# Kernel optimization log

Measured on AMD Instinct MI355X. Metric: run time of the kernel, lower is better.

The kernel has to match this reference:

```python
import jax, jax.numpy as jnp
import numpy as np

D = 128      # d_model
H = 8        # nhead
DFF = 256    # dim_feedforward
S = 1000     # num sets
L = 90       # set size
N = S * L    # total tokens (lidar voxels + image patches)
VN = 45000   # voxel_num (lidar tokens)


def _ln(x, g, b, eps=1e-5):
    m = x.mean(-1, keepdims=True)
    v = ((x - m) ** 2).mean(-1, keepdims=True)
    return (x - m) / jnp.sqrt(v + eps) * g + b


def setup_inputs() -> dict:
    key = jax.random.key(0)
    ks = jax.random.split(key, 16)
    p = lambda k, sh: jax.random.normal(k, sh, jnp.float32) * 0.02
    inp = {
        "src": jax.random.normal(ks[0], (N, D), jnp.float32),
        "pos": jax.random.normal(ks[1], (N, D), jnp.float32),
        # every token appears exactly once across all sets (permutation)
        "set_voxel_inds": jax.random.permutation(ks[2], N).reshape(S, L).astype(jnp.int32),
        "set_voxel_masks": jnp.zeros((S, L), bool),
        "voxel_num": VN,
        # nn.MultiheadAttention params
        "in_proj_w": p(ks[3], (3 * D, D)), "in_proj_b": jnp.zeros((3 * D,), jnp.float32),
        "out_w": p(ks[4], (D, D)), "out_b": jnp.zeros((D,), jnp.float32),
        # image-branch FFN + norms
        "lin1_w": p(ks[5], (DFF, D)), "lin1_b": jnp.zeros((DFF,), jnp.float32),
        "lin2_w": p(ks[6], (D, DFF)), "lin2_b": jnp.zeros((D,), jnp.float32),
        "n1_g": jnp.ones((D,), jnp.float32), "n1_b": jnp.zeros((D,), jnp.float32),
        "n2_g": jnp.ones((D,), jnp.float32), "n2_b": jnp.zeros((D,), jnp.float32),
        # lidar-branch FFN + norms (split_ffn=True)
        "l_lin1_w": p(ks[7], (DFF, D)), "l_lin1_b": jnp.zeros((DFF,), jnp.float32),
        "l_lin2_w": p(ks[8], (D, DFF)), "l_lin2_b": jnp.zeros((D,), jnp.float32),
        "ln1_g": jnp.ones((D,), jnp.float32), "ln1_b": jnp.zeros((D,), jnp.float32),
        "ln2_g": jnp.ones((D,), jnp.float32), "ln2_b": jnp.zeros((D,), jnp.float32),
        # encoder-layer output norm
        "enc_g": jnp.ones((D,), jnp.float32), "enc_b": jnp.zeros((D,), jnp.float32),
    }
    return inp


def reference(src, pos, set_voxel_inds, set_voxel_masks, voxel_num,
              in_proj_w, in_proj_b, out_w, out_b,
              lin1_w, lin1_b, lin2_w, lin2_b, n1_g, n1_b, n2_g, n2_b,
              l_lin1_w, l_lin1_b, l_lin2_w, l_lin2_b, ln1_g, ln1_b, ln2_g, ln2_b,
              enc_g, enc_b):
    identity = src
    Sx, Lx = set_voxel_inds.shape
    d = src.shape[-1]
    dh = d // H

    # ---- gather sets ----
    sf = src[set_voxel_inds]              # [S, L, D]
    sp = pos[set_voxel_inds]              # [S, L, D]
    q = sf + sp
    k = sf + sp
    v = sf

    # ---- nn.MultiheadAttention (batch_first, eval mode) ----
    qp = q @ in_proj_w[:d].T + in_proj_b[:d]
    kp = k @ in_proj_w[d:2 * d].T + in_proj_b[d:2 * d]
    vp = v @ in_proj_w[2 * d:].T + in_proj_b[2 * d:]
    qh = qp.reshape(Sx, Lx, H, dh)
    kh = kp.reshape(Sx, Lx, H, dh)
    vh = vp.reshape(Sx, Lx, H, dh)
    scale = 1.0 / np.sqrt(dh).astype(np.float32)
    scores = jnp.einsum('sqhd,skhd->shqk', qh, kh) * scale
    scores = scores + jnp.where(set_voxel_masks[:, None, None, :], -1e9, 0.0)
    attn = jax.nn.softmax(scores, axis=-1)
    o = jnp.einsum('shqk,skhd->sqhd', attn, vh).reshape(Sx, Lx, d)
    src2 = o @ out_w.T + out_b            # [S, L, D]

    # ---- scatter back to per-token order (first-occurrence via flip trick) ----
    flat = set_voxel_inds.reshape(-1)
    ar = jnp.arange(flat.shape[0], dtype=flat.dtype)
    perm = jnp.zeros((src.shape[0],), flat.dtype).at[flat[::-1]].set(ar[::-1])
    src2 = src2.reshape(-1, d)[perm]      # [N, D]

    # ---- split FFN (lidar first voxel_num tokens, image rest) ----
    x = src + src2
    x = jnp.concatenate([_ln(x[:voxel_num], ln1_g, ln1_b),
                         _ln(x[voxel_num:], n1_g, n1_b)], axis=0)
    fl = jax.nn.relu(x[:voxel_num] @ l_lin1_w.T + l_lin1_b) @ l_lin2_w.T + l_lin2_b
    fi = jax.nn.relu(x[voxel_num:] @ lin1_w.T + lin1_b) @ lin2_w.T + lin2_b
    x = x + jnp.concatenate([fl, fi], axis=0)
    x = jnp.concatenate([_ln(x[:voxel_num], ln2_g, ln2_b),
                         _ln(x[voxel_num:], n2_g, n2_b)], axis=0)

    # ---- UniTR_EncoderLayer residual + final norm ----
    return _ln(x + identity, enc_g, enc_b)
```

## Files before the change

### kernel.cpp

```cpp
#include <hip/hip_runtime.h>
#include <hip/hip_bf16.h>
#include <cmath>

#define N_TOK 90000
#define DM 128
#define NH 8
#define DH 16
#define NS 1000
#define LS 90
#define LSP 96
#define DFF 256
#define VN 45000
#define NB_L 704
#define NB_I 704

typedef __attribute__((ext_vector_type(8))) short short8;
typedef __attribute__((ext_vector_type(4))) short short4_t;
typedef __attribute__((ext_vector_type(4))) float f32x4;

#define SWZ(row, byte) ((byte) ^ (((row) & 7) << 4))

__device__ __forceinline__ unsigned short f2bf(float f) {
  __hip_bfloat16 h = __float2bfloat16(f);
  union { __hip_bfloat16 h; unsigned short u; } c; c.h = h; return c.u;
}
__device__ __forceinline__ float bf2f(unsigned short u) {
  union { unsigned short u; __hip_bfloat16 h; } c; c.u = u; return __bfloat162float(c.h);
}

__global__ __launch_bounds__(256) void k_wconv(
    const float* __restrict__ a0, const float* __restrict__ a1,
    const float* __restrict__ a2, const float* __restrict__ a3,
    const float* __restrict__ a4, const float* __restrict__ a5,
    unsigned short* __restrict__ dst)
{
  int c = blockIdx.x * 256 + threadIdx.x;
  const float* s; int base, kkn, K;
  if      (c <  6144) { s = a0; base = 0;     kkn = 4; K = 128; }
  else if (c <  8192) { s = a1; base = 6144;  kkn = 4; K = 128; }
  else if (c < 12288) { s = a2; base = 8192;  kkn = 4; K = 128; }
  else if (c < 16384) { s = a3; base = 12288; kkn = 4; K = 128; }
  else if (c < 20480) { s = a4; base = 16384; kkn = 8; K = 256; }
  else                { s = a5; base = 20480; kkn = 8; K = 256; }
  int lc = c - base;
  int nt = lc / (kkn * 64);
  int rem = lc - nt * (kkn * 64);
  int kk = rem >> 6, l = rem & 63;
  int row = nt * 16 + (l & 15);
  int col = kk * 32 + (l >> 4) * 8;
  const float* sp = s + (size_t)row * K + col;
  short8 o;
  #pragma unroll
  for (int e = 0; e < 8; e++) o[e] = (short)f2bf(sp[e]);
  *(short8*)&dst[(size_t)c * 8] = o;
}

__global__ __launch_bounds__(512, 4) void k_set(
    const float* __restrict__ src, const float* __restrict__ pos,
    const int* __restrict__ inds, const unsigned char* __restrict__ masks,
    const unsigned short* __restrict__ Wq, const float* __restrict__ bq_,
    const unsigned short* __restrict__ Wo, const float* __restrict__ bo,
    const float* __restrict__ lg, const float* __restrict__ lb,
    const float* __restrict__ ig, const float* __restrict__ ib,
    unsigned short* __restrict__ x1)
{
  __shared__ __align__(16) char QKV[LSP * 256 + 128 * 200];
  __shared__ float bias[LSP];
  __shared__ int tok[LSP];
  const int s = blockIdx.x;
  const int tid = threadIdx.x;
  const int w = tid >> 6, l = tid & 63;
  const int g = l >> 4, cb = l & 15;

  char* Kd = QKV;
  char* Vt = QKV + LSP * 256;
  char* Qd = QKV + LSP * 256;

  const int row = w * 16 + cb;
  short8 bq[4];

  if (tid >= 384 && tid < 384 + LSP) {
    int i = tid - 384;
    tok[i] = inds[s * LS + ((i < LS) ? i : 0)];
    bias[i] = (i < LS && !masks[s * LS + i]) ? 0.f : -1e9f;
  }

  if (w < 6) {
    const int t = inds[s * LS + ((row < LS) ? row : 0)];
    short8 bv[4];
    #pragma unroll
    for (int kk = 0; kk < 4; kk++) {
      const float* sp = &src[(size_t)t * DM + kk * 32 + g * 8];
      const float* pp = &pos[(size_t)t * DM + kk * 32 + g * 8];
      float4 s0 = *(const float4*)sp, s1 = *(const float4*)(sp + 4);
      float4 p0 = *(const float4*)pp, p1 = *(const float4*)(pp + 4);
      short8 q, v;
      q[0] = (short)f2bf(s0.x + p0.x); q[1] = (short)f2bf(s0.y + p0.y);
      q[2] = (short)f2bf(s0.z + p0.z); q[3] = (short)f2bf(s0.w + p0.w);
      q[4] = (short)f2bf(s1.x + p1.x); q[5] = (short)f2bf(s1.y + p1.y);
      q[6] = (short)f2bf(s1.z + p1.z); q[7] = (short)f2bf(s1.w + p1.w);
      v[0] = (short)f2bf(s0.x); v[1] = (short)f2bf(s0.y);
      v[2] = (short)f2bf(s0.z); v[3] = (short)f2bf(s0.w);
      v[4] = (short)f2bf(s1.x); v[5] = (short)f2bf(s1.y);
      v[6] = (short)f2bf(s1.z); v[7] = (short)f2bf(s1.w);
      bq[kk] = q; bv[kk] = v;
    }

    #pragma unroll
    for (int nt = 16; nt < 24; nt++) {
      const unsigned short* wb = Wq + ((size_t)nt * 256 + l) * 8;
      short8 A[4];
      #pragma unroll
      for (int kk = 0; kk < 4; kk++) A[kk] = *(const short8*)(wb + kk * 512);
      f32x4 acc = {0.f, 0.f, 0.f, 0.f};
      #pragma unroll
      for (int kk = 0; kk < 4; kk++)
        acc = __builtin_amdgcn_mfma_f32_16x16x32_bf16(A[kk], bv[kk], acc, 0, 0, 0);
      float4 bb = *(const float4*)&bq_[nt * 16 + g * 4];
      float bba[4] = {bb.x, bb.y, bb.z, bb.w};
      #pragma unroll
      for (int j = 0; j < 4; j++) {
        int ch = (nt - 16) * 16 + g * 4 + j;
        *(unsigned short*)(Vt + ch * 200 + row * 2) = f2bf(acc[j] + bba[j]);
      }
    }

    #pragma unroll
    for (int nt = 8; nt < 16; nt++) {
      const unsigned short* wb = Wq + ((size_t)nt * 256 + l) * 8;
      short8 A[4];
      #pragma unroll
      for (int kk = 0; kk < 4; kk++) A[kk] = *(const short8*)(wb + kk * 512);
      f32x4 acc = {0.f, 0.f, 0.f, 0.f};
      #pragma unroll
      for (int kk = 0; kk < 4; kk++)
        acc = __builtin_amdgcn_mfma_f32_16x16x32_bf16(A[kk], bq[kk], acc, 0, 0, 0);
      float4 bb = *(const float4*)&bq_[nt * 16 + g * 4];
      const int colb = (nt & 7) * 16 + g * 4;
      short4_t o;
      o[0] = (short)f2bf(acc[0] + bb.x); o[1] = (short)f2bf(acc[1] + bb.y);
      o[2] = (short)f2bf(acc[2] + bb.z); o[3] = (short)f2bf(acc[3] + bb.w);
      *(short4_t*)(Kd + SWZ(row, row * 256 + colb * 2)) = o;
    }
  }
  __syncthreads();

  short8 aV[3];
  #pragma unroll
  for (int kb = 0; kb < 3; kb++) {
    const char* vr = Vt + (w * 16 + cb) * 200;
    short4_t lo = *(const short4_t*)(vr + (kb * 32 + g * 4) * 2);
    short4_t hi = *(const short4_t*)(vr + (kb * 32 + 16 + g * 4) * 2);
    short8 v;
    v[0] = lo[0]; v[1] = lo[1]; v[2] = lo[2]; v[3] = lo[3];
    v[4] = hi[0]; v[5] = hi[1]; v[6] = hi[2]; v[7] = hi[3];
    aV[kb] = v;
  }
  __syncthreads();

  if (w < 6) {
    #pragma unroll
    for (int nt = 0; nt < 8; nt++) {
      const unsigned short* wb = Wq + ((size_t)nt * 256 + l) * 8;
      short8 A[4];
      #pragma unroll
      for (int kk = 0; kk < 4; kk++) A[kk] = *(const short8*)(wb + kk * 512);
      f32x4 acc = {0.f, 0.f, 0.f, 0.f};
      #pragma unroll
      for (int kk = 0; kk < 4; kk++)
        acc = __builtin_amdgcn_mfma_f32_16x16x32_bf16(A[kk], bq[kk], acc, 0, 0, 0);
      float4 bb = *(const float4*)&bq_[nt * 16 + g * 4];
      const int colb = nt * 16 + g * 4;
      short4_t o;
      o[0] = (short)f2bf(acc[0] + bb.x); o[1] = (short)f2bf(acc[1] + bb.y);
      o[2] = (short)f2bf(acc[2] + bb.z); o[3] = (short)f2bf(acc[3] + bb.w);
      *(short4_t*)(Qd + SWZ(row, row * 256 + colb * 2)) = o;
    }
  }
  __syncthreads();

  {
    const int hb = w * 32;
    float bi[6][4];
    #pragma unroll
    for (int kt = 0; kt < 6; kt++)
      #pragma unroll
      for (int r = 0; r < 4; r++)
        bi[kt][r] = bias[kt * 16 + g * 4 + r];

    short8 aK[6];
    #pragma unroll
    for (int kt = 0; kt < 6; kt++) {
      short8 v = {0, 0, 0, 0, 0, 0, 0, 0};
      int key = kt * 16 + cb;
      if (g < 2) v = *(const short8*)(Kd + SWZ(key, key * 256 + hb + g * 16));
      aK[kt] = v;
    }

    #pragma unroll
    for (int qt = 0; qt < 6; qt++) {
      const int qi = qt * 16 + cb;
      short8 aQ = {0, 0, 0, 0, 0, 0, 0, 0};
      if (g < 2) aQ = *(const short8*)(Qd + SWZ(qi, qi * 256 + hb + g * 16));

      f32x4 acc[6];
      #pragma unroll
      for (int kt = 0; kt < 6; kt++) {
        f32x4 z = {0.f, 0.f, 0.f, 0.f};
        acc[kt] = __builtin_amdgcn_mfma_f32_16x16x32_bf16(aK[kt], aQ, z, 0, 0, 0);
      }
      #pragma unroll
      for (int kt = 0; kt < 6; kt++)
        #pragma unroll
        for (int r = 0; r < 4; r++)
          acc[kt][r] = acc[kt][r] * 0.25f + bi[kt][r];
      float mx = -1e30f;
      #pragma unroll
      for (int kt = 0; kt < 6; kt++)
        #pragma unroll
        for (int r = 0; r < 4; r++) mx = fmaxf(mx, acc[kt][r]);
      mx = fmaxf(mx, __shfl_xor(mx, 16));
      mx = fmaxf(mx, __shfl_xor(mx, 32));
      float sm = 0.f;
      #pragma unroll
      for (int kt = 0; kt < 6; kt++)
        #pragma unroll
        for (int r = 0; r < 4; r++) {
          acc[kt][r] = __expf(acc[kt][r] - mx);
          sm += acc[kt][r];
        }
      sm += __shfl_xor(sm, 16);
      sm += __shfl_xor(sm, 32);
      const float inv = 1.f / sm;
      f32x4 accO = {0.f, 0.f, 0.f, 0.f};
      #pragma unroll
      for (int kb = 0; kb < 3; kb++) {
        short8 p;
        #pragma unroll
        for (int e = 0; e < 8; e++) {
          int kt = kb * 2 + (e >> 2);
          p[e] = (short)f2bf(acc[kt][e & 3] * inv);
        }
        accO = __builtin_amdgcn_mfma_f32_16x16x32_bf16(aV[kb], p, accO, 0, 0, 0);
      }
      if (qi < LS) {
        short4_t o;
        #pragma unroll
        for (int r = 0; r < 4; r++) o[r] = (short)f2bf(accO[r]);
        *(short4_t*)(Qd + SWZ(qi, qi * 256 + hb + g * 8)) = o;
      }
    }
  }
  __syncthreads();

  if (w < 6) {
    const bool ok = row < LS;
    const int t = tok[row];
    short8 bf[4];
    #pragma unroll
    for (int kk = 0; kk < 4; kk++)
      bf[kk] = *(const short8*)(Qd + SWZ(row, row * 256 + kk * 64 + g * 16));

    float ta[8][4]; float ssum = 0.f;
    #pragma unroll
    for (int nt = 0; nt < 8; nt++) {
      const unsigned short* wb = Wo + ((size_t)nt * 256 + l) * 8;
      short8 A[4];
      #pragma unroll
      for (int kk = 0; kk < 4; kk++) A[kk] = *(const short8*)(wb + kk * 512);
      f32x4 c = {0.f, 0.f, 0.f, 0.f};
      #pragma unroll
      for (int kk = 0; kk < 4; kk++)
        c = __builtin_amdgcn_mfma_f32_16x16x32_bf16(A[kk], bf[kk], c, 0, 0, 0);
      float4 bo4 = *(const float4*)&bo[nt * 16 + g * 4];
      float4 sv  = *(const float4*)&src[(size_t)t * DM + nt * 16 + g * 4];
      ta[nt][0] = c[0] + bo4.x + sv.x;
      ta[nt][1] = c[1] + bo4.y + sv.y;
      ta[nt][2] = c[2] + bo4.z + sv.z;
      ta[nt][3] = c[3] + bo4.w + sv.w;
      ssum += ta[nt][0] + ta[nt][1] + ta[nt][2] + ta[nt][3];
    }
    ssum += __shfl_xor(ssum, 16); ssum += __shfl_xor(ssum, 32);
    const float mean = ssum * (1.f / 128.f);
    float vv = 0.f;
    #pragma unroll
    for (int nt = 0; nt < 8; nt++)
      #pragma unroll
      for (int j = 0; j < 4; j++) { float d = ta[nt][j] - mean; vv += d * d; }
    vv += __shfl_xor(vv, 16); vv += __shfl_xor(vv, 32);
    const float rstd = rsqrtf(vv * (1.f / 128.f) + 1e-5f);
    const bool lidar = t < VN;
    const float* gp = lidar ? lg : ig;
    const float* bp = lidar ? lb : ib;
    #pragma unroll
    for (int nt = 0; nt < 8; nt++) {
      float4 g4 = *(const float4*)&gp[nt * 16 + g * 4];
      float4 b4 = *(const float4*)&bp[nt * 16 + g * 4];
      short4_t o;
      o[0] = (short)f2bf((ta[nt][0] - mean) * rstd * g4.x + b4.x);
      o[1] = (short)f2bf((ta[nt][1] - mean) * rstd * g4.y + b4.y);
      o[2] = (short)f2bf((ta[nt][2] - mean) * rstd * g4.z + b4.z);
      o[3] = (short)f2bf((ta[nt][3] - mean) * rstd * g4.w + b4.w);
      if (ok) *(short4_t*)&x1[(size_t)t * DM + nt * 16 + g * 4] = o;
    }
  }
}

__global__ __launch_bounds__(256) void k_ffn(
    const unsigned short* __restrict__ x1, const float* __restrict__ src,
    const unsigned short* __restrict__ W1l, const float* __restrict__ B1l,
    const unsigned short* __restrict__ W1i, const float* __restrict__ B1i,
    const unsigned short* __restrict__ W2l, const float* __restrict__ B2l,
    const unsigned short* __restrict__ W2i, const float* __restrict__ B2i,
    const float* __restrict__ lg2, const float* __restrict__ lbb2,
    const float* __restrict__ ig2, const float* __restrict__ ibb2,
    const float* __restrict__ eg, const float* __restrict__ eb,
    float* __restrict__ out)
{
  __shared__ __align__(16) unsigned short hid[64 * 256];
  const int tid = threadIdx.x;
  const int w = tid >> 6, l = tid & 63;
  const int g = l >> 4, cb = l & 15;
  const bool lid = blockIdx.x < NB_L;
  const int t0 = lid ? blockIdx.x * 64 : VN + (blockIdx.x - NB_L) * 64;
  const int limit = lid ? VN : N_TOK;
  const unsigned short* W1 = lid ? W1l : W1i;
  const float* B1 = lid ? B1l : B1i;
  const unsigned short* W2 = lid ? W2l : W2i;
  const float* B2 = lid ? B2l : B2i;
  const float* g2  = lid ? lg2  : ig2;
  const float* bb2 = lid ? lbb2 : ibb2;

  const int row = w * 16 + cb;
  const int t = t0 + row;
  const int tc = (t < limit) ? t : (limit - 1);
  const bool ok = t < limit;

  short8 b1[4];
  #pragma unroll
  for (int kk = 0; kk < 4; kk++)
    b1[kk] = *(const short8*)&x1[(size_t)tc * DM + kk * 32 + g * 8];

  for (int nt = 0; nt < 16; nt++) {
    const unsigned short* wbase = W1 + ((size_t)nt * 256 + l) * 8;
    short8 A[4];
    #pragma unroll
    for (int kk = 0; kk < 4; kk++) A[kk] = *(const short8*)(wbase + kk * 512);
    f32x4 acc = {0.f, 0.f, 0.f, 0.f};
    #pragma unroll
    for (int kk = 0; kk < 4; kk++)
      acc = __builtin_amdgcn_mfma_f32_16x16x32_bf16(A[kk], b1[kk], acc, 0, 0, 0);
    float4 bb = *(const float4*)&B1[nt * 16 + g * 4];
    short4_t h;
    h[0] = (short)f2bf(fmaxf(acc[0] + bb.x, 0.f));
    h[1] = (short)f2bf(fmaxf(acc[1] + bb.y, 0.f));
    h[2] = (short)f2bf(fmaxf(acc[2] + bb.z, 0.f));
    h[3] = (short)f2bf(fmaxf(acc[3] + bb.w, 0.f));
    *(short4_t*)((char*)hid + SWZ(row, row * 512 + nt * 32 + g * 8)) = h;
  }

  short8 b2[8];
  #pragma unroll
  for (int kk = 0; kk < 8; kk++)
    b2[kk] = *(const short8*)((const char*)hid + SWZ(row, row * 512 + kk * 64 + g * 16));

  f32x4 acc2[8];
  for (int nt = 0; nt < 8; nt++) {
    const unsigned short* wbase = W2 + ((size_t)nt * 512 + l) * 8;
    short8 A[8];
    #pragma unroll
    for (int kk = 0; kk < 8; kk++) A[kk] = *(const short8*)(wbase + kk * 512);
    f32x4 c = {0.f, 0.f, 0.f, 0.f};
    #pragma unroll
    for (int kk = 0; kk < 8; kk++)
      c = __builtin_amdgcn_mfma_f32_16x16x32_bf16(A[kk], b2[kk], c, 0, 0, 0);
    acc2[nt] = c;
  }

  float ta[8][4]; float s = 0.f;
  #pragma unroll
  for (int nt = 0; nt < 8; nt++) {
    short4_t xv = *(const short4_t*)&x1[(size_t)tc * DM + nt * 16 + g * 4];
    float4 bb = *(const float4*)&B2[nt * 16 + g * 4];
    ta[nt][0] = bf2f((unsigned short)xv[0]) + acc2[nt][0] + bb.x;
    ta[nt][1] = bf2f((unsigned short)xv[1]) + acc2[nt][1] + bb.y;
    ta[nt][2] = bf2f((unsigned short)xv[2]) + acc2[nt][2] + bb.z;
    ta[nt][3] = bf2f((unsigned short)xv[3]) + acc2[nt][3] + bb.w;
    s += ta[nt][0] + ta[nt][1] + ta[nt][2] + ta[nt][3];
  }
  s += __shfl_xor(s, 16); s += __shfl_xor(s, 32);
  const float mean = s * (1.f / 128.f);
  float vv = 0.f;
  #pragma unroll
  for (int nt = 0; nt < 8; nt++)
    #pragma unroll
    for (int j = 0; j < 4; j++) { float d = ta[nt][j] - mean; vv += d * d; }
  vv += __shfl_xor(vv, 16); vv += __shfl_xor(vv, 32);
  const float rstd = rsqrtf(vv * (1.f / 128.f) + 1e-5f);

  float za[8][4]; float s2 = 0.f;
  #pragma unroll
  for (int nt = 0; nt < 8; nt++) {
    float4 g4 = *(const float4*)&g2[nt * 16 + g * 4];
    float4 b4 = *(const float4*)&bb2[nt * 16 + g * 4];
    float4 sv = *(const float4*)&src[(size_t)tc * DM + nt * 16 + g * 4];
    za[nt][0] = (ta[nt][0] - mean) * rstd * g4.x + b4.x + sv.x;
    za[nt][1] = (ta[nt][1] - mean) * rstd * g4.y + b4.y + sv.y;
    za[nt][2] = (ta[nt][2] - mean) * rstd * g4.z + b4.z + sv.z;
    za[nt][3] = (ta[nt][3] - mean) * rstd * g4.w + b4.w + sv.w;
    s2 += za[nt][0] + za[nt][1] + za[nt][2] + za[nt][3];
  }
  s2 += __shfl_xor(s2, 16); s2 += __shfl_xor(s2, 32);
  const float mean2 = s2 * (1.f / 128.f);
  float vv2 = 0.f;
  #pragma unroll
  for (int nt = 0; nt < 8; nt++)
    #pragma unroll
    for (int j = 0; j < 4; j++) { float d = za[nt][j] - mean2; vv2 += d * d; }
  vv2 += __shfl_xor(vv2, 16); vv2 += __shfl_xor(vv2, 32);
  const float rstd2 = rsqrtf(vv2 * (1.f / 128.f) + 1e-5f);

  #pragma unroll
  for (int nt = 0; nt < 8; nt++) {
    float4 e4 = *(const float4*)&eg[nt * 16 + g * 4];
    float4 eb4 = *(const float4*)&eb[nt * 16 + g * 4];
    float4 o;
    o.x = (za[nt][0] - mean2) * rstd2 * e4.x + eb4.x;
    o.y = (za[nt][1] - mean2) * rstd2 * e4.y + eb4.y;
    o.z = (za[nt][2] - mean2) * rstd2 * e4.z + eb4.z;
    o.w = (za[nt][3] - mean2) * rstd2 * e4.w + eb4.w;
    if (ok) *(float4*)&out[(size_t)t * DM + nt * 16 + g * 4] = o;
  }
}

extern "C" void kernel_launch(void* const* d_in, const int* in_sizes, int n_in,
                              void* d_out, int out_size, void* d_ws, size_t ws_size,
                              hipStream_t stream) {
  (void)in_sizes; (void)n_in; (void)out_size;
  const float* src  = (const float*)d_in[0];
  const float* pos  = (const float*)d_in[1];
  const int*   inds = (const int*)d_in[2];
  const unsigned char* masks = (const unsigned char*)d_in[3];
  const float* Wqkv = (const float*)d_in[5];
  const float* bqkv = (const float*)d_in[6];
  const float* Wo   = (const float*)d_in[7];
  const float* bo   = (const float*)d_in[8];
  const float* lin1_w = (const float*)d_in[9];
  const float* lin1_b = (const float*)d_in[10];
  const float* lin2_w = (const float*)d_in[11];
  const float* lin2_b = (const float*)d_in[12];
  const float* n1_g = (const float*)d_in[13];
  const float* n1_b = (const float*)d_in[14];
  const float* n2_g = (const float*)d_in[15];
  const float* n2_b = (const float*)d_in[16];
  const float* l_lin1_w = (const float*)d_in[17];
  const float* l_lin1_b = (const float*)d_in[18];
  const float* l_lin2_w = (const float*)d_in[19];
  const float* l_lin2_b = (const float*)d_in[20];
  const float* ln1_g = (const float*)d_in[21];
  const float* ln1_b = (const float*)d_in[22];
  const float* ln2_g = (const float*)d_in[23];
  const float* ln2_b = (const float*)d_in[24];
  const float* enc_g = (const float*)d_in[25];
  const float* enc_b = (const float*)d_in[26];

  const size_t buf = (size_t)N_TOK * DM;
  if (ws_size < (buf + 196608) * sizeof(unsigned short)) return;
  unsigned short* x1  = (unsigned short*)d_ws;
  unsigned short* Wbf = x1 + buf;
  unsigned short* WbQKV = Wbf;
  unsigned short* WbO   = Wbf + 6144  * 8;
  unsigned short* Wb1L  = Wbf + 8192  * 8;
  unsigned short* Wb1I  = Wbf + 12288 * 8;
  unsigned short* Wb2L  = Wbf + 16384 * 8;
  unsigned short* Wb2I  = Wbf + 20480 * 8;

  k_wconv<<<96, 256, 0, stream>>>(Wqkv, Wo, l_lin1_w, lin1_w, l_lin2_w, lin2_w, Wbf);
  k_set<<<NS, 512, 0, stream>>>(src, pos, inds, masks, WbQKV, bqkv, WbO, bo,
                                ln1_g, ln1_b, n1_g, n1_b, x1);
  k_ffn<<<NB_L + NB_I, 256, 0, stream>>>(x1, src,
                                         Wb1L, l_lin1_b, Wb1I, lin1_b,
                                         Wb2L, l_lin2_b, Wb2I, lin2_b,
                                         ln2_g, ln2_b, n2_g, n2_b,
                                         enc_g, enc_b, (float*)d_out);
}
```

Baseline: 135.9 us.

## Split QKV projection into its own kernel and move out-proj into FFN kernel

Splits the fused set-attention kernel into three stages. A token-ordered QKV projection kernel writes bf16 Q/K/V to a workspace buffer. The attention kernel then only gathers Q/K/V by set indices and writes per-token attention outputs. The output projection and first LayerNorm move into the FFN kernel. This gives coalesced, contiguous-token GEMMs instead of gathered rows and lightens the attention kernel, at the cost of an extra launch and a 90000x384 bf16 intermediate round trip through memory.

```diff
diff --git a/kernel.cpp b/kernel.cpp
--- a/kernel.cpp
+++ b/kernel.cpp
@@ -13,6 +13,7 @@
 #define VN 45000
 #define NB_L 704
 #define NB_I 704
+#define NBQ 1407
 
 typedef __attribute__((ext_vector_type(8))) short short8;
 typedef __attribute__((ext_vector_type(4))) short short4_t;
@@ -55,16 +56,78 @@
   *(short8*)&dst[(size_t)c * 8] = o;
 }
 
-__global__ __launch_bounds__(512, 4) void k_set(
+__global__ __launch_bounds__(256) void k_qkv(
     const float* __restrict__ src, const float* __restrict__ pos,
+    const unsigned short* __restrict__ Wq, const float* __restrict__ bq_,
+    unsigned short* __restrict__ qkv)
+{
+  const int tid = threadIdx.x;
+  const int w = tid >> 6, l = tid & 63;
+  const int g = l >> 4, cb = l & 15;
+  const int row = w * 16 + cb;
+  const int t = blockIdx.x * 64 + row;
+  const int tc = (t < N_TOK) ? t : (N_TOK - 1);
+  const bool ok = t < N_TOK;
+
+  short8 bq[4], bv[4];
+  #pragma unroll
+  for (int kk = 0; kk < 4; kk++) {
+    const float* sp = &src[(size_t)tc * DM + kk * 32 + g * 8];
+    const float* pp = &pos[(size_t)tc * DM + kk * 32 + g * 8];
+    float4 s0 = *(const float4*)sp, s1 = *(const float4*)(sp + 4);
+    float4 p0 = *(const float4*)pp, p1 = *(const float4*)(pp + 4);
+    short8 q, v;
+    q[0] = (short)f2bf(s0.x + p0.x); q[1] = (short)f2bf(s0.y + p0.y);
+    q[2] = (short)f2bf(s0.z + p0.z); q[3] = (short)f2bf(s0.w + p0.w);
+    q[4] = (short)f2bf(s1.x + p1.x); q[5] = (short)f2bf(s1.y + p1.y);
+    q[6] = (short)f2bf(s1.z + p1.z); q[7] = (short)f2bf(s1.w + p1.w);
+    v[0] = (short)f2bf(s0.x); v[1] = (short)f2bf(s0.y);
+    v[2] = (short)f2bf(s0.z); v[3] = (short)f2bf(s0.w);
+    v[4] = (short)f2bf(s1.x); v[5] = (short)f2bf(s1.y);
+    v[6] = (short)f2bf(s1.z); v[7] = (short)f2bf(s1.w);
+    bq[kk] = q; bv[kk] = v;
+  }
+
+  #pragma unroll
+  for (int nt = 0; nt < 16; nt++) {
+    const unsigned short* wb = Wq + ((size_t)nt * 256 + l) * 8;
+    short8 A[4];
+    #pragma unroll
+    for (int kk = 0; kk < 4; kk++) A[kk] = *(const short8*)(wb + kk * 512);
+    f32x4 acc = {0.f, 0.f, 0.f, 0.f};
+    #pragma unroll
+    for (int kk = 0; kk < 4; kk++)
+      acc = __builtin_amdgcn_mfma_f32_16x16x32_bf16(A[kk], bq[kk], acc, 0, 0, 0);
+    float4 bb = *(const float4*)&bq_[nt * 16 + g * 4];
+    short4_t o;
+    o[0] = (short)f2bf(acc[0] + bb.x); o[1] = (short)f2bf(acc[1] + bb.y);
+    o[2] = (short)f2bf(acc[2] + bb.z); o[3] = (short)f2bf(acc[3] + bb.w);
+    if (ok) *(short4_t*)&qkv[(size_t)t * 384 + nt * 16 + g * 4] = o;
+  }
+  #pragma unroll
+  for (int nt = 16; nt < 24; nt++) {
+    const unsigned short* wb = Wq + ((size_t)nt * 256 + l) * 8;
+    short8 A[4];
+    #pragma unroll
+    for (int kk = 0; kk < 4; kk++) A[kk] = *(const short8*)(wb + kk * 512);
+    f32x4 acc = {0.f, 0.f, 0.f, 0.f};
+    #pragma unroll
+    for (int kk = 0; kk < 4; kk++)
+      acc = __builtin_amdgcn_mfma_f32_16x16x32_bf16(A[kk], bv[kk], acc, 0, 0, 0);
+    float4 bb = *(const float4*)&bq_[nt * 16 + g * 4];
+    short4_t o;
+    o[0] = (short)f2bf(acc[0] + bb.x); o[1] = (short)f2bf(acc[1] + bb.y);
+    o[2] = (short)f2bf(acc[2] + bb.z); o[3] = (short)f2bf(acc[3] + bb.w);
+    if (ok) *(short4_t*)&qkv[(size_t)t * 384 + nt * 16 + g * 4] = o;
+  }
+}
+
+__global__ __launch_bounds__(512, 4) void k_attn(
+    const unsigned short* __restrict__ qkv,
     const int* __restrict__ inds, const unsigned char* __restrict__ masks,
-    const unsigned short* __restrict__ Wq, const float* __restrict__ bq_,
-    const unsigned short* __restrict__ Wo, const float* __restrict__ bo,
-    const float* __restrict__ lg, const float* __restrict__ lb,
-    const float* __restrict__ ig, const float* __restrict__ ib,
-    unsigned short* __restrict__ x1)
+    unsigned short* __restrict__ obuf)
 {
-  __shared__ __align__(16) char QKV[LSP * 256 + 128 * 200];
+  __shared__ __align__(16) char SM[LSP * 256 + 128 * 200];
   __shared__ float bias[LSP];
   __shared__ int tok[LSP];
   const int s = blockIdx.x;
@@ -72,9 +135,9 @@
   const int w = tid >> 6, l = tid & 63;
   const int g = l >> 4, cb = l & 15;
 
-  char* Kd = QKV;
-  char* Vt = QKV + LSP * 256;
-  char* Qd = QKV + LSP * 256;
+  char* Kd = SM;
+  char* Vt = SM + LSP * 256;
+  char* Qd = SM + LSP * 256;
 
   const int row = w * 16 + cb;
   short8 bq[4];
@@ -87,61 +150,24 @@
 
   if (w < 6) {
     const int t = inds[s * LS + ((row < LS) ? row : 0)];
-    short8 bv[4];
+    const unsigned short* qr = qkv + (size_t)t * 384;
     #pragma unroll
     for (int kk = 0; kk < 4; kk++) {
-      const float* sp = &src[(size_t)t * DM + kk * 32 + g * 8];
-      const float* pp = &pos[(size_t)t * DM + kk * 32 + g * 8];
-      float4 s0 = *(const float4*)sp, s1 = *(const float4*)(sp + 4);
-      float4 p0 = *(const float4*)pp, p1 = *(const float4*)(pp + 4);
-      short8 q, v;
-      q[0] = (short)f2bf(s0.x + p0.x); q[1] = (short)f2bf(s0.y + p0.y);
-      q[2] = (short)f2bf(s0.z + p0.z); q[3] = (short)f2bf(s0.w + p0.w);
-      q[4] = (short)f2bf(s1.x + p1.x); q[5] = (short)f2bf(s1.y + p1.y);
-      q[6] = (short)f2bf(s1.z + p1.z); q[7] = (short)f2bf(s1.w + p1.w);
-      v[0] = (short)f2bf(s0.x); v[1] = (short)f2bf(s0.y);
-      v[2] = (short)f2bf(s0.z); v[3] = (short)f2bf(s0.w);
-      v[4] = (short)f2bf(s1.x); v[5] = (short)f2bf(s1.y);
-      v[6] = (short)f2bf(s1.z); v[7] = (short)f2bf(s1.w);
-      bq[kk] = q; bv[kk] = v;
+      short8 kv = *(const short8*)(qr + 128 + kk * 32 + g * 8);
+      *(short8*)(Kd + SWZ(row, row * 256 + kk * 64 + g * 16)) = kv;
     }
-
-    #pragma unroll
-    for (int nt = 16; nt < 24; nt++) {
-      const unsigned short* wb = Wq + ((size_t)nt * 256 + l) * 8;
-      short8 A[4];
-      #pragma unroll
-      for (int kk = 0; kk < 4; kk++) A[kk] = *(const short8*)(wb + kk * 512);
-      f32x4 acc = {0.f, 0.f, 0.f, 0.f};
-      #pragma unroll
-      for (int kk = 0; kk < 4; kk++)
-        acc = __builtin_amdgcn_mfma_f32_16x16x32_bf16(A[kk], bv[kk], acc, 0, 0, 0);
-      float4 bb = *(const float4*)&bq_[nt * 16 + g * 4];
-      float bba[4] = {bb.x, bb.y, bb.z, bb.w};
-      #pragma unroll
-      for (int j = 0; j < 4; j++) {
-        int ch = (nt - 16) * 16 + g * 4 + j;
-        *(unsigned short*)(Vt + ch * 200 + row * 2) = f2bf(acc[j] + bba[j]);
+    #pragma unroll
+    for (int kk = 0; kk < 4; kk++) {
+      short8 vv = *(const short8*)(qr + 256 + kk * 32 + g * 8);
+      #pragma unroll
+      for (int e = 0; e < 8; e++) {
+        int ch = kk * 32 + g * 8 + e;
+        *(unsigned short*)(Vt + ch * 200 + row * 2) = (unsigned short)vv[e];
       }
     }
-
-    #pragma unroll
-    for (int nt = 8; nt < 16; nt++) {
-      const unsigned short* wb = Wq + ((size_t)nt * 256 + l) * 8;
-      short8 A[4];
-      #pragma unroll
-      for (int kk = 0; kk < 4; kk++) A[kk] = *(const short8*)(wb + kk * 512);
-      f32x4 acc = {0.f, 0.f, 0.f, 0.f};
-      #pragma unroll
-      for (int kk = 0; kk < 4; kk++)
-        acc = __builtin_amdgcn_mfma_f32_16x16x32_bf16(A[kk], bq[kk], acc, 0, 0, 0);
-      float4 bb = *(const float4*)&bq_[nt * 16 + g * 4];
-      const int colb = (nt & 7) * 16 + g * 4;
-      short4_t o;
-      o[0] = (short)f2bf(acc[0] + bb.x); o[1] = (short)f2bf(acc[1] + bb.y);
-      o[2] = (short)f2bf(acc[2] + bb.z); o[3] = (short)f2bf(acc[3] + bb.w);
-      *(short4_t*)(Kd + SWZ(row, row * 256 + colb * 2)) = o;
-    }
+    #pragma unroll
+    for (int kk = 0; kk < 4; kk++)
+      bq[kk] = *(const short8*)(qr + kk * 32 + g * 8);
   }
   __syncthreads();
 
@@ -160,22 +186,8 @@
 
   if (w < 6) {
     #pragma unroll
-    for (int nt = 0; nt < 8; nt++) {
-      const unsigned short* wb = Wq + ((size_t)nt * 256 + l) * 8;
-      short8 A[4];
-      #pragma unroll
-      for (int kk = 0; kk < 4; kk++) A[kk] = *(const short8*)(wb + kk * 512);
-      f32x4 acc = {0.f, 0.f, 0.f, 0.f};
-      #pragma unroll
-      for (int kk = 0; kk < 4; kk++)
-        acc = __builtin_amdgcn_mfma_f32_16x16x32_bf16(A[kk], bq[kk], acc, 0, 0, 0);
-      float4 bb = *(const float4*)&bq_[nt * 16 + g * 4];
-      const int colb = nt * 16 + g * 4;
-      short4_t o;
-      o[0] = (short)f2bf(acc[0] + bb.x); o[1] = (short)f2bf(acc[1] + bb.y);
-      o[2] = (short)f2bf(acc[2] + bb.z); o[3] = (short)f2bf(acc[3] + bb.w);
-      *(short4_t*)(Qd + SWZ(row, row * 256 + colb * 2)) = o;
-    }
+    for (int kk = 0; kk < 4; kk++)
+      *(short8*)(Qd + SWZ(row, row * 256 + kk * 64 + g * 16)) = bq[kk];
   }
   __syncthreads();
 
@@ -253,65 +265,25 @@
   }
   __syncthreads();
 
-  if (w < 6) {
-    const bool ok = row < LS;
+  if (w < 6 && row < LS) {
     const int t = tok[row];
-    short8 bf[4];
-    #pragma unroll
-    for (int kk = 0; kk < 4; kk++)
-      bf[kk] = *(const short8*)(Qd + SWZ(row, row * 256 + kk * 64 + g * 16));
-
-    float ta[8][4]; float ssum = 0.f;
-    #pragma unroll
-    for (int nt = 0; nt < 8; nt++) {
-      const unsigned short* wb = Wo + ((size_t)nt * 256 + l) * 8;
-      short8 A[4];
-      #pragma unroll
-      for (int kk = 0; kk < 4; kk++) A[kk] = *(const short8*)(wb + kk * 512);
-      f32x4 c = {0.f, 0.f, 0.f, 0.f};
-      #pragma unroll
-      for (int kk = 0; kk < 4; kk++)
-        c = __builtin_amdgcn_mfma_f32_16x16x32_bf16(A[kk], bf[kk], c, 0, 0, 0);
-      float4 bo4 = *(const float4*)&bo[nt * 16 + g * 4];
-      float4 sv  = *(const float4*)&src[(size_t)t * DM + nt * 16 + g * 4];
-      ta[nt][0] = c[0] + bo4.x + sv.x;
-      ta[nt][1] = c[1] + bo4.y + sv.y;
-      ta[nt][2] = c[2] + bo4.z + sv.z;
-      ta[nt][3] = c[3] + bo4.w + sv.w;
-      ssum += ta[nt][0] + ta[nt][1] + ta[nt][2] + ta[nt][3];
+    #pragma unroll
+    for (int kk = 0; kk < 4; kk++) {
+      short8 ov = *(const short8*)(Qd + SWZ(row, row * 256 + kk * 64 + g * 16));
+      *(short8*)&obuf[(size_t)t * DM + kk * 32 + g * 8] = ov;
     }
-    ssum += __shfl_xor(ssum, 16); ssum += __shfl_xor(ssum, 32);
-    const float mean = ssum * (1.f / 128.f);
-    float vv = 0.f;
-    #pragma unroll
-    for (int nt = 0; nt < 8; nt++)
-      #pragma unroll
-      for (int j = 0; j < 4; j++) { float d = ta[nt][j] - mean; vv += d * d; }
-    vv += __shfl_xor(vv, 16); vv += __shfl_xor(vv, 32);
-    const float rstd = rsqrtf(vv * (1.f / 128.f) + 1e-5f);
-    const bool lidar = t < VN;
-    const float* gp = lidar ? lg : ig;
-    const float* bp = lidar ? lb : ib;
-    #pragma unroll
-    for (int nt = 0; nt < 8; nt++) {
-      float4 g4 = *(const float4*)&gp[nt * 16 + g * 4];
-      float4 b4 = *(const float4*)&bp[nt * 16 + g * 4];
-      short4_t o;
-      o[0] = (short)f2bf((ta[nt][0] - mean) * rstd * g4.x + b4.x);
-      o[1] = (short)f2bf((ta[nt][1] - mean) * rstd * g4.y + b4.y);
-      o[2] = (short)f2bf((ta[nt][2] - mean) * rstd * g4.z + b4.z);
-      o[3] = (short)f2bf((ta[nt][3] - mean) * rstd * g4.w + b4.w);
-      if (ok) *(short4_t*)&x1[(size_t)t * DM + nt * 16 + g * 4] = o;
-    }
   }
 }
 
 __global__ __launch_bounds__(256) void k_ffn(
-    const unsigned short* __restrict__ x1, const float* __restrict__ src,
+    const unsigned short* __restrict__ obuf, const float* __restrict__ src,
+    const unsigned short* __restrict__ Wo, const float* __restrict__ bo,
     const unsigned short* __restrict__ W1l, const float* __restrict__ B1l,
     const unsigned short* __restrict__ W1i, const float* __restrict__ B1i,
     const unsigned short* __restrict__ W2l, const float* __restrict__ B2l,
     const unsigned short* __restrict__ W2i, const float* __restrict__ B2i,
+    const float* __restrict__ lg1, const float* __restrict__ lb1,
+    const float* __restrict__ ig1, const float* __restrict__ ib1,
     const float* __restrict__ lg2, const float* __restrict__ lbb2,
     const float* __restrict__ ig2, const float* __restrict__ ibb2,
     const float* __restrict__ eg, const float* __restrict__ eb,
@@ -328,6 +300,8 @@
   const float* B1 = lid ? B1l : B1i;
   const unsigned short* W2 = lid ? W2l : W2i;
   const float* B2 = lid ? B2l : B2i;
+  const float* g1  = lid ? lg1  : ig1;
+  const float* bb1 = lid ? lb1  : ib1;
   const float* g2  = lid ? lg2  : ig2;
   const float* bb2 = lid ? lbb2 : ibb2;
 
@@ -336,10 +310,58 @@
   const int tc = (t < limit) ? t : (limit - 1);
   const bool ok = t < limit;
 
+  short8 b0[4];
+  #pragma unroll
+  for (int kk = 0; kk < 4; kk++)
+    b0[kk] = *(const short8*)&obuf[(size_t)tc * DM + kk * 32 + g * 8];
+
+  float ta[8][4]; float ssum = 0.f;
+  #pragma unroll
+  for (int nt = 0; nt < 8; nt++) {
+    const unsigned short* wb = Wo + ((size_t)nt * 256 + l) * 8;
+    short8 A[4];
+    #pragma unroll
+    for (int kk = 0; kk < 4; kk++) A[kk] = *(const short8*)(wb + kk * 512);
+    f32x4 c = {0.f, 0.f, 0.f, 0.f};
+    #pragma unroll
+    for (int kk = 0; kk < 4; kk++)
+      c = __builtin_amdgcn_mfma_f32_16x16x32_bf16(A[kk], b0[kk], c, 0, 0, 0);
+    float4 bo4 = *(const float4*)&bo[nt * 16 + g * 4];
+    float4 sv  = *(const float4*)&src[(size_t)tc * DM + nt * 16 + g * 4];
+    ta[nt][0] = c[0] + bo4.x + sv.x;
+    ta[nt][1] = c[1] + bo4.y + sv.y;
+    ta[nt][2] = c[2] + bo4.z + sv.z;
+    ta[nt][3] = c[3] + bo4.w + sv.w;
+    ssum += ta[nt][0] + ta[nt][1] + ta[nt][2] + ta[nt][3];
+  }
+  ssum += __shfl_xor(ssum, 16); ssum += __shfl_xor(ssum, 32);
+  const float mean1 = ssum * (1.f / 128.f);
+  float vv1 = 0.f;
+  #pragma unroll
+  for (int nt = 0; nt < 8; nt++)
+    #pragma unroll
+    for (int j = 0; j < 4; j++) { float d = ta[nt][j] - mean1; vv1 += d * d; }
+  vv1 += __shfl_xor(vv1, 16); vv1 += __shfl_xor(vv1, 32);
+  const float rstd1 = rsqrtf(vv1 * (1.f / 128.f) + 1e-5f);
+
+  short4_t xb[8];
+  #pragma unroll
+  for (int nt = 0; nt < 8; nt++) {
+    float4 g4 = *(const float4*)&g1[nt * 16 + g * 4];
+    float4 b4 = *(const float4*)&bb1[nt * 16 + g * 4];
+    short4_t o;
+    o[0] = (short)f2bf((ta[nt][0] - mean1) * rstd1 * g4.x + b4.x);
+    o[1] = (short)f2bf((ta[nt][1] - mean1) * rstd1 * g4.y + b4.y);
+    o[2] = (short)f2bf((ta[nt][2] - mean1) * rstd1 * g4.z + b4.z);
+    o[3] = (short)f2bf((ta[nt][3] - mean1) * rstd1 * g4.w + b4.w);
+    xb[nt] = o;
+    *(short4_t*)((char*)hid + SWZ(row, row * 256 + nt * 32 + g * 8)) = o;
+  }
   short8 b1[4];
   #pragma unroll
   for (int kk = 0; kk < 4; kk++)
-    b1[kk] = *(const short8*)&x1[(size_t)tc * DM + kk * 32 + g * 8];
+    b1[kk] = *(const short8*)((const char*)hid + SWZ(row, row * 256 + kk * 64 + g * 16));
+  __syncthreads();
 
   for (int nt = 0; nt < 16; nt++) {
     const unsigned short* wbase = W1 + ((size_t)nt * 256 + l) * 8;
@@ -377,16 +399,15 @@
     acc2[nt] = c;
   }
 
-  float ta[8][4]; float s = 0.f;
+  float ta2[8][4]; float s = 0.f;
   #pragma unroll
   for (int nt = 0; nt < 8; nt++) {
-    short4_t xv = *(const short4_t*)&x1[(size_t)tc * DM + nt * 16 + g * 4];
     float4 bb = *(const float4*)&B2[nt * 16 + g * 4];
-    ta[nt][0] = bf2f((unsigned short)xv[0]) + acc2[nt][0] + bb.x;
-    ta[nt][1] = bf2f((unsigned short)xv[1]) + acc2[nt][1] + bb.y;
-    ta[nt][2] = bf2f((unsigned short)xv[2]) + acc2[nt][2] + bb.z;
-    ta[nt][3] = bf2f((unsigned short)xv[3]) + acc2[nt][3] + bb.w;
-    s += ta[nt][0] + ta[nt][1] + ta[nt][2] + ta[nt][3];
+    ta2[nt][0] = bf2f((unsigned short)xb[nt][0]) + acc2[nt][0] + bb.x;
+    ta2[nt][1] = bf2f((unsigned short)xb[nt][1]) + acc2[nt][1] + bb.y;
+    ta2[nt][2] = bf2f((unsigned short)xb[nt][2]) + acc2[nt][2] + bb.z;
+    ta2[nt][3] = bf2f((unsigned short)xb[nt][3]) + acc2[nt][3] + bb.w;
+    s += ta2[nt][0] + ta2[nt][1] + ta2[nt][2] + ta2[nt][3];
   }
   s += __shfl_xor(s, 16); s += __shfl_xor(s, 32);
   const float mean = s * (1.f / 128.f);
@@ -394,7 +415,7 @@
   #pragma unroll
   for (int nt = 0; nt < 8; nt++)
     #pragma unroll
-    for (int j = 0; j < 4; j++) { float d = ta[nt][j] - mean; vv += d * d; }
+    for (int j = 0; j < 4; j++) { float d = ta2[nt][j] - mean; vv += d * d; }
   vv += __shfl_xor(vv, 16); vv += __shfl_xor(vv, 32);
   const float rstd = rsqrtf(vv * (1.f / 128.f) + 1e-5f);
 
@@ -404,10 +425,10 @@
     float4 g4 = *(const float4*)&g2[nt * 16 + g * 4];
     float4 b4 = *(const float4*)&bb2[nt * 16 + g * 4];
     float4 sv = *(const float4*)&src[(size_t)tc * DM + nt * 16 + g * 4];
-    za[nt][0] = (ta[nt][0] - mean) * rstd * g4.x + b4.x + sv.x;
-    za[nt][1] = (ta[nt][1] - mean) * rstd * g4.y + b4.y + sv.y;
-    za[nt][2] = (ta[nt][2] - mean) * rstd * g4.z + b4.z + sv.z;
-    za[nt][3] = (ta[nt][3] - mean) * rstd * g4.w + b4.w + sv.w;
+    za[nt][0] = (ta2[nt][0] - mean) * rstd * g4.x + b4.x + sv.x;
+    za[nt][1] = (ta2[nt][1] - mean) * rstd * g4.y + b4.y + sv.y;
+    za[nt][2] = (ta2[nt][2] - mean) * rstd * g4.z + b4.z + sv.z;
+    za[nt][3] = (ta2[nt][3] - mean) * rstd * g4.w + b4.w + sv.w;
     s2 += za[nt][0] + za[nt][1] + za[nt][2] + za[nt][3];
   }
   s2 += __shfl_xor(s2, 16); s2 += __shfl_xor(s2, 32);
@@ -464,10 +485,12 @@
   const float* enc_g = (const float*)d_in[25];
   const float* enc_b = (const float*)d_in[26];
 
-  const size_t buf = (size_t)N_TOK * DM;
-  if (ws_size < (buf + 196608) * sizeof(unsigned short)) return;
-  unsigned short* x1  = (unsigned short*)d_ws;
-  unsigned short* Wbf = x1 + buf;
+  const size_t nObuf = (size_t)N_TOK * DM;
+  const size_t nQkv  = (size_t)N_TOK * 384;
+  if (ws_size < (nObuf + nQkv + 196608) * sizeof(unsigned short)) return;
+  unsigned short* obuf = (unsigned short*)d_ws;
+  unsigned short* qkvb = obuf + nObuf;
+  unsigned short* Wbf  = qkvb + nQkv;
   unsigned short* WbQKV = Wbf;
   unsigned short* WbO   = Wbf + 6144  * 8;
   unsigned short* Wb1L  = Wbf + 8192  * 8;
@@ -476,11 +499,13 @@
   unsigned short* Wb2I  = Wbf + 20480 * 8;
 
   k_wconv<<<96, 256, 0, stream>>>(Wqkv, Wo, l_lin1_w, lin1_w, l_lin2_w, lin2_w, Wbf);
-  k_set<<<NS, 512, 0, stream>>>(src, pos, inds, masks, WbQKV, bqkv, WbO, bo,
-                                ln1_g, ln1_b, n1_g, n1_b, x1);
-  k_ffn<<<NB_L + NB_I, 256, 0, stream>>>(x1, src,
+  k_qkv<<<NBQ, 256, 0, stream>>>(src, pos, WbQKV, bqkv, qkvb);
+  k_attn<<<NS, 512, 0, stream>>>(qkvb, inds, masks, obuf);
+  k_ffn<<<NB_L + NB_I, 256, 0, stream>>>(obuf, src,
+                                         WbO, bo,
                                          Wb1L, l_lin1_b, Wb1I, lin1_b,
                                          Wb2L, l_lin2_b, Wb2I, lin2_b,
+                                         ln1_g, ln1_b, n1_g, n1_b,
                                          ln2_g, ln2_b, n2_g, n2_b,
                                          enc_g, enc_b, (float*)d_out);
 }
```

New measurement: 179.4 us. 1.32x slower.
